# Kernel optimization log

Hardware: AMD Instinct MI355X
Metric: run time of the kernel (lower is better)

## Reference

```python
import jax, jax.numpy as jnp
import numpy as np
import math

NUM_WORDS = 8192
WORD_WIDTH = 512
PROJ_WIDTH = 64
NUM_HEADS = 8
SCALE_FACTOR = 100.0

def setup_inputs() -> dict:
    key = jax.random.key(0)
    kx, kq, kk, kv, ko = jax.random.split(key, 5)
    x = jax.random.normal(kx, (NUM_WORDS, WORD_WIDTH), dtype=jnp.float32)
    w_q = jax.random.normal(kq, (WORD_WIDTH, PROJ_WIDTH), dtype=jnp.float32) / SCALE_FACTOR
    w_k = jax.random.normal(kk, (WORD_WIDTH, PROJ_WIDTH), dtype=jnp.float32) / SCALE_FACTOR
    w_v = jax.random.normal(kv, (WORD_WIDTH, PROJ_WIDTH), dtype=jnp.float32) / SCALE_FACTOR
    w_o = jax.random.normal(ko, (WORD_WIDTH, WORD_WIDTH), dtype=jnp.float32)
    return {"x": x, "w_q": w_q, "w_k": w_k, "w_v": w_v, "w_o": w_o}

def reference(x, w_q, w_k, w_v, w_o):
    # Single self-attention head (all 8 heads in the source share the same weights).
    q = x @ w_q            # [N, P]
    k = x @ w_k            # [N, P]
    v = x @ w_v            # [N, P]
    scores = jax.nn.softmax((q @ k.T) / jnp.sqrt(jnp.float32(q.shape[1])), axis=1)  # [N, N]
    head = scores @ v      # [N, P]
    # concat of NUM_HEADS identical head outputs along dim=1
    concat = jnp.tile(head, (1, NUM_HEADS))  # [N, NUM_HEADS*P]
    return concat @ w_o    # [N, WORD_WIDTH]
```

## Files before the change

kernel.cpp:

```cpp
#include <hip/hip_runtime.h>
#include <stdint.h>

#define N_WORDS 8192
#define LOG2E_8 0.18033688011112043f

typedef __attribute__((ext_vector_type(8))) short short8;
typedef __attribute__((ext_vector_type(4))) float f32x4;
typedef __attribute__((ext_vector_type(16))) float f32x16;
typedef __attribute__((ext_vector_type(2))) __fp16 pkhalf2;
typedef __attribute__((ext_vector_type(4))) _Float16 half4;
typedef __attribute__((ext_vector_type(8))) _Float16 half8;

__device__ __forceinline__ unsigned short f32_to_bf16(float f) {
    union { float f; unsigned u; } v; v.f = f;
    unsigned u = v.u;
    return (unsigned short)((u + 0x7FFFu + ((u >> 16) & 1u)) >> 16);
}

__device__ __forceinline__ unsigned short f32_to_f16(float f) {
    union { _Float16 h; unsigned short u; } cv;
    cv.h = (_Float16)f;
    return cv.u;
}

__device__ __forceinline__ void async16(const void* g, void* l) {
    __builtin_amdgcn_global_load_lds(
        (const __attribute__((address_space(1))) unsigned int*)g,
        (__attribute__((address_space(3))) unsigned int*)l, 16, 0, 0);
}

__global__ __launch_bounds__(256) void qkv_gemm(
    const float* __restrict__ x,
    const float* __restrict__ wq, const float* __restrict__ wk,
    const float* __restrict__ wv, const float* __restrict__ wo,
    unsigned short* __restrict__ qB, unsigned short* __restrict__ kB,
    unsigned short* __restrict__ vH, unsigned short* __restrict__ weT)
{
    int t = threadIdx.x;
    int mat = blockIdx.y;

    if (mat == 3) {
        int i = blockIdx.x * 256 + t;
        int p = i >> 9;
        int j = i & 511;
        float s = 0.0f;
#pragma unroll
        for (int h = 0; h < 8; ++h) s += wo[(size_t)(h * 64 + p) * 512 + j];
        weT[(size_t)j * 64 + p] = f32_to_f16(s);
        return;
    }

    __shared__ __align__(16) unsigned short ldsX[64 * 72];
    __shared__ __align__(16) unsigned short ldsW[64 * 72];

    int mt = blockIdx.x;
    const float* w = (mat == 0) ? wq : (mat == 1) ? wk : wv;

    int wvid = t >> 6, lane = t & 63;
    int lq = lane & 15, quad = lane >> 4;

    f32x4 acc[4];
#pragma unroll
    for (int nt = 0; nt < 4; ++nt) acc[nt] = (f32x4){0.f, 0.f, 0.f, 0.f};

    float4 xr[4];
    float wr[16];
    int wn = t & 63, wkbs = (t >> 6) * 16;

    {
#pragma unroll
        for (int j2 = 0; j2 < 4; ++j2) {
            int i = t + j2 * 256;
            int row = i >> 4, c4 = (i & 15) * 4;
            xr[j2] = *(const float4*)(x + (size_t)(mt * 64 + row) * 512 + c4);
        }
#pragma unroll
        for (int kk = 0; kk < 16; ++kk)
            wr[kk] = w[(size_t)(wkbs + kk) * 64 + wn];
    }

    for (int kb = 0; kb < 8; ++kb) {
        __syncthreads();
#pragma unroll
        for (int j2 = 0; j2 < 4; ++j2) {
            int i = t + j2 * 256;
            int row = i >> 4, c4 = (i & 15) * 4;
            unsigned p0 = f32_to_bf16(xr[j2].x) | ((unsigned)f32_to_bf16(xr[j2].y) << 16);
            unsigned p1 = f32_to_bf16(xr[j2].z) | ((unsigned)f32_to_bf16(xr[j2].w) << 16);
            *(uint2*)(&ldsX[row * 72 + c4]) = make_uint2(p0, p1);
        }
#pragma unroll
        for (int kk = 0; kk < 16; kk += 2) {
            unsigned p = f32_to_bf16(wr[kk]) | ((unsigned)f32_to_bf16(wr[kk + 1]) << 16);
            *(unsigned*)(&ldsW[wn * 72 + wkbs + kk]) = p;
        }
        __syncthreads();

        if (kb < 7) {
            int k0 = (kb + 1) * 64;
#pragma unroll
            for (int j2 = 0; j2 < 4; ++j2) {
                int i = t + j2 * 256;
                int row = i >> 4, c4 = (i & 15) * 4;
                xr[j2] = *(const float4*)(x + (size_t)(mt * 64 + row) * 512 + k0 + c4);
            }
#pragma unroll
            for (int kk = 0; kk < 16; ++kk)
                wr[kk] = w[(size_t)(k0 + wkbs + kk) * 64 + wn];
        }

        int m = wvid * 16 + lq;
        short8 a0 = *(const short8*)(&ldsX[m * 72 + quad * 8]);
        short8 a1 = *(const short8*)(&ldsX[m * 72 + 32 + quad * 8]);
#pragma unroll
        for (int nt = 0; nt < 4; ++nt) {
            short8 b0 = *(const short8*)(&ldsW[(nt * 16 + lq) * 72 + quad * 8]);
            short8 b1 = *(const short8*)(&ldsW[(nt * 16 + lq) * 72 + 32 + quad * 8]);
            acc[nt] = __builtin_amdgcn_mfma_f32_16x16x32_bf16(a0, b0, acc[nt], 0, 0, 0);
            acc[nt] = __builtin_amdgcn_mfma_f32_16x16x32_bf16(a1, b1, acc[nt], 0, 0, 0);
        }
    }

    int mrow_base = mt * 64 + wvid * 16;
#pragma unroll
    for (int nt = 0; nt < 4; ++nt) {
#pragma unroll
        for (int r = 0; r < 4; ++r) {
            int row = mrow_base + quad * 4 + r;
            int n = nt * 16 + lq;
            float v = acc[nt][r];
            if (mat == 0) {
                v *= LOG2E_8;
                int col = ((((n >> 3) ^ (row & 7)) << 3)) | (n & 7);
                qB[(size_t)row * 64 + col] = f32_to_bf16(v);
            } else if (mat == 1) {
                int col = ((((n >> 3) ^ (row & 7)) << 3)) | (n & 7);
                kB[(size_t)row * 64 + col] = f32_to_bf16(v);
            } else {
                int rs = (row & ~63) | (((((row >> 3) & 7) ^ (n & 7)) << 3)) | (row & 7);
                vH[(size_t)n * N_WORDS + rs] = f32_to_f16(v);
            }
        }
    }
}

__global__ __launch_bounds__(256) void attn_kernel(
    const unsigned short* __restrict__ qB,
    const unsigned short* __restrict__ kB,
    const unsigned short* __restrict__ vH,
    unsigned short* __restrict__ pOh, float* __restrict__ pl,
    int nk, int sshift)
{
    __shared__ __align__(16) unsigned short ldsK[2][128 * 64];
    __shared__ __align__(16) unsigned short ldsV[2][64 * 128];

    int t = threadIdx.x;
    int bid = blockIdx.x;
    int s = bid & ((1 << sshift) - 1);
    int qb = bid >> sshift;
    int wvid = t >> 6, lane = t & 63;
    int l31 = lane & 31, hi = lane >> 5;
    int mbase = qb * 128 + wvid * 32;
    int n0 = s * nk;

    short8 qf[4];
    {
        int qrow = mbase + l31;
        const unsigned short* qr = qB + (size_t)qrow * 64;
        int s7 = qrow & 7;
#pragma unroll
        for (int c = 0; c < 4; ++c)
            qf[c] = *(const short8*)(qr + (((2 * c + hi) ^ s7) << 3));
    }

    f32x16 zero16;
#pragma unroll
    for (int i = 0; i < 16; ++i) zero16[i] = 0.f;
    f32x16 oacc[2];
    oacc[0] = zero16;
    oacc[1] = zero16;
    float lsum = 0.f;

    auto stage = [&](int buf, int nb) {
        const char* gK = (const char*)kB + (size_t)nb * 128;
#pragma unroll
        for (int i = 0; i < 4; ++i) {
            int L0 = (wvid * 4 + i) * 64;
            async16(gK + (size_t)(L0 + lane) * 16, (char*)ldsK[buf] + (size_t)L0 * 16);
        }
#pragma unroll
        for (int i = 0; i < 4; ++i) {
            int L0 = (wvid * 4 + i) * 64;
            int L = L0 + lane;
            int vcol = L >> 4, ct = L & 15;
            const char* src = (const char*)vH + (size_t)vcol * 16384 +
                              (size_t)nb * 2 + ((ct >> 3) << 7) + ((ct & 7) << 4);
            async16(src, (char*)ldsV[buf] + (size_t)L0 * 16);
        }
    };

    int tiles = nk >> 7;
    stage(0, n0);
    int cur = 0;

    for (int tt = 0; tt < tiles; ++tt) {
        __syncthreads();
        if (tt + 1 < tiles) stage(cur ^ 1, n0 + (tt + 1) * 128);

        __builtin_amdgcn_s_setprio(1);
        const unsigned short* K = ldsK[cur];
        const unsigned short* V = ldsV[cur];

#pragma unroll
        for (int nt = 0; nt < 4; ++nt) {
            const unsigned short* kr = K + (nt * 32 + l31) * 64;
            int s7 = l31 & 7;
            f32x16 st = zero16;
#pragma unroll
            for (int c = 0; c < 4; ++c) {
                short8 a = *(const short8*)(kr + (((2 * c + hi) ^ s7) << 3));
                st = __builtin_amdgcn_mfma_f32_32x32x16_bf16(a, qf[c], st, 0, 0, 0);
            }

            union { half8 v8[2]; pkhalf2 v2[8]; } pa;
#pragma unroll
            for (int p = 0; p < 8; ++p) {
                float e0 = exp2f(st[2 * p]);
                float e1 = exp2f(st[2 * p + 1]);
                lsum += e0 + e1;
                pa.v2[p] = __builtin_amdgcn_cvt_pkrtz(e0, e1);
            }

#pragma unroll
            for (int m = 0; m < 2; ++m) {
                int c0 = 4 * nt + 2 * m;
                int c1 = c0 + 1;
#pragma unroll
                for (int vt = 0; vt < 2; ++vt) {
                    int vcol = vt * 32 + l31;
                    int cs0 = (c0 & 8) | ((c0 & 7) ^ (vcol & 7));
                    int cs1 = (c1 & 8) | ((c1 & 7) ^ (vcol & 7));
                    union { half8 v8; half4 v4[2]; } vb;
                    vb.v4[0] = *(const half4*)(V + vcol * 128 + (cs0 << 3) + hi * 4);
                    vb.v4[1] = *(const half4*)(V + vcol * 128 + (cs1 << 3) + hi * 4);
                    oacc[vt] = __builtin_amdgcn_mfma_f32_32x32x16_f16(
                        pa.v8[m], vb.v8, oacc[vt], 0, 0, 0);
                }
            }
        }
        __builtin_amdgcn_s_setprio(0);
        cur ^= 1;
    }

    lsum += __shfl_xor(lsum, 32);

    size_t obase = (size_t)s * N_WORDS;
    if (hi == 0) pl[obase + mbase + l31] = lsum;

    __syncthreads();
    unsigned short* ldsO = &ldsK[0][0];
#pragma unroll
    for (int vt = 0; vt < 2; ++vt)
#pragma unroll
        for (int r = 0; r < 16; ++r) {
            int lrow = wvid * 32 + (r & 3) + 8 * (r >> 2) + 4 * hi;
            ldsO[lrow * 64 + vt * 32 + l31] = f32_to_f16(oacc[vt][r]);
        }
    __syncthreads();
    {
        const uint4* U = (const uint4*)ldsO;
        uint4* G = (uint4*)(pOh + (obase + (size_t)qb * 128) * 64);
#pragma unroll
        for (int j = 0; j < 4; ++j)
            G[t + 256 * j] = U[t + 256 * j];
    }
}

__global__ __launch_bounds__(256) void out_kernel(
    const unsigned short* __restrict__ pOh, const float* __restrict__ pl,
    const unsigned short* __restrict__ weT, float* __restrict__ out, int S)
{
    __shared__ __align__(16) _Float16 ldsH[16 * 72];
    int t = threadIdx.x;
    int r0 = blockIdx.x * 16;
    const _Float16* pOf = (const _Float16*)pOh;

#pragma unroll
    for (int j = 0; j < 4; ++j) {
        int i = t + j * 256;
        int row = i >> 6, d = i & 63;
        float so = 0.f, sl = 0.f;
        for (int s = 0; s < S; ++s) {
            so += (float)pOf[((size_t)s * N_WORDS + r0 + row) * 64 + d];
            sl += pl[(size_t)s * N_WORDS + r0 + row];
        }
        ldsH[row * 72 + d] = (_Float16)(so / sl);
    }
    __syncthreads();

    int wv = t >> 6, lane = t & 63;
    int lq = lane & 15, quad = lane >> 4;

    half8 a0 = *(const half8*)(&ldsH[lq * 72 + quad * 8]);
    half8 a1 = *(const half8*)(&ldsH[lq * 72 + 32 + quad * 8]);
    const _Float16* wT = (const _Float16*)weT;

#pragma unroll
    for (int ntl = 0; ntl < 8; ++ntl) {
        int nt = wv * 8 + ntl;
        const _Float16* wrow = wT + (size_t)(nt * 16 + lq) * 64;
        half8 b0 = *(const half8*)(wrow + quad * 8);
        half8 b1 = *(const half8*)(wrow + 32 + quad * 8);
        f32x4 acc = (f32x4){0.f, 0.f, 0.f, 0.f};
        acc = __builtin_amdgcn_mfma_f32_16x16x32_f16(a0, b0, acc, 0, 0, 0);
        acc = __builtin_amdgcn_mfma_f32_16x16x32_f16(a1, b1, acc, 0, 0, 0);
#pragma unroll
        for (int r = 0; r < 4; ++r)
            out[(size_t)(r0 + quad * 4 + r) * 512 + nt * 16 + lq] = acc[r];
    }
}

extern "C" void kernel_launch(void* const* d_in, const int* in_sizes, int n_in,
                              void* d_out, int out_size, void* d_ws, size_t ws_size,
                              hipStream_t stream)
{
    const float* x  = (const float*)d_in[0];
    const float* wq = (const float*)d_in[1];
    const float* wk = (const float*)d_in[2];
    const float* wv = (const float*)d_in[3];
    const float* wo = (const float*)d_in[4];
    float* out = (float*)d_out;

    char* ws = (char*)d_ws;
    unsigned short* qB  = (unsigned short*)(ws);
    unsigned short* kB  = (unsigned short*)(ws + 1048576);
    unsigned short* vH  = (unsigned short*)(ws + 2097152);
    unsigned short* weT = (unsigned short*)(ws + 3145728);
    float* pl           = (float*)(ws + 3211264);
    unsigned short* pOh = (unsigned short*)(ws + 3735552);

    size_t base = 3735552;
    int S = (ws_size >= base + 8u * 1048576u) ? 8 : 4;
    int sshift = (S == 8) ? 3 : 2;
    int nk = N_WORDS / S;

    hipLaunchKernelGGL(qkv_gemm, dim3(128, 4), dim3(256), 0, stream,
                       x, wq, wk, wv, wo, qB, kB, vH, weT);
    hipLaunchKernelGGL(attn_kernel, dim3(64 * S), dim3(256), 0, stream,
                       qB, kB, vH, pOh, pl, nk, sshift);
    hipLaunchKernelGGL(out_kernel, dim3(512), dim3(256), 0, stream,
                       pOh, pl, weT, out, S);
}
```

Before: 129.8 us.

## Process two query groups per wave to reuse K/V tiles, raise key splits

Each wave in the attention kernel now handles 64 query rows, as two 32-row groups, instead of 32. Every K and V fragment read from LDS feeds two MFMAs, which halves LDS read traffic per query and gives more independent MFMAs to interleave. To keep the grid size, the key-split count rises to 16 when the workspace is large enough, so each block walks fewer key tiles. The cost is roughly doubled accumulator and Q register usage, and more partial results for the output kernel to combine.

```diff
diff --git a/kernel.cpp b/kernel.cpp
--- a/kernel.cpp
+++ b/kernel.cpp
@@ -144,7 +144,7 @@
     }
 }
 
-__global__ __launch_bounds__(256) void attn_kernel(
+__global__ __launch_bounds__(256, 2) void attn_kernel(
     const unsigned short* __restrict__ qB,
     const unsigned short* __restrict__ kB,
     const unsigned short* __restrict__ vH,
@@ -160,26 +160,27 @@
     int qb = bid >> sshift;
     int wvid = t >> 6, lane = t & 63;
     int l31 = lane & 31, hi = lane >> 5;
-    int mbase = qb * 128 + wvid * 32;
+    int mbase = qb * 256 + wvid * 64;
     int n0 = s * nk;
 
-    short8 qf[4];
-    {
-        int qrow = mbase + l31;
+    short8 qf[2][4];
+#pragma unroll
+    for (int qg = 0; qg < 2; ++qg) {
+        int qrow = mbase + qg * 32 + l31;
         const unsigned short* qr = qB + (size_t)qrow * 64;
         int s7 = qrow & 7;
 #pragma unroll
         for (int c = 0; c < 4; ++c)
-            qf[c] = *(const short8*)(qr + (((2 * c + hi) ^ s7) << 3));
+            qf[qg][c] = *(const short8*)(qr + (((2 * c + hi) ^ s7) << 3));
     }
 
     f32x16 zero16;
 #pragma unroll
     for (int i = 0; i < 16; ++i) zero16[i] = 0.f;
-    f32x16 oacc[2];
-    oacc[0] = zero16;
-    oacc[1] = zero16;
-    float lsum = 0.f;
+    f32x16 oacc[2][2];
+    oacc[0][0] = zero16; oacc[0][1] = zero16;
+    oacc[1][0] = zero16; oacc[1][1] = zero16;
+    float lsum0 = 0.f, lsum1 = 0.f;
 
     auto stage = [&](int buf, int nb) {
         const char* gK = (const char*)kB + (size_t)nb * 128;
@@ -215,20 +216,31 @@
         for (int nt = 0; nt < 4; ++nt) {
             const unsigned short* kr = K + (nt * 32 + l31) * 64;
             int s7 = l31 & 7;
-            f32x16 st = zero16;
-#pragma unroll
-            for (int c = 0; c < 4; ++c) {
-                short8 a = *(const short8*)(kr + (((2 * c + hi) ^ s7) << 3));
-                st = __builtin_amdgcn_mfma_f32_32x32x16_bf16(a, qf[c], st, 0, 0, 0);
-            }
-
-            union { half8 v8[2]; pkhalf2 v2[8]; } pa;
+            short8 a0 = *(const short8*)(kr + (((0 + hi) ^ s7) << 3));
+            short8 a1 = *(const short8*)(kr + (((2 + hi) ^ s7) << 3));
+            short8 a2 = *(const short8*)(kr + (((4 + hi) ^ s7) << 3));
+            short8 a3 = *(const short8*)(kr + (((6 + hi) ^ s7) << 3));
+            f32x16 st0 = zero16, st1 = zero16;
+            st0 = __builtin_amdgcn_mfma_f32_32x32x16_bf16(a0, qf[0][0], st0, 0, 0, 0);
+            st1 = __builtin_amdgcn_mfma_f32_32x32x16_bf16(a0, qf[1][0], st1, 0, 0, 0);
+            st0 = __builtin_amdgcn_mfma_f32_32x32x16_bf16(a1, qf[0][1], st0, 0, 0, 0);
+            st1 = __builtin_amdgcn_mfma_f32_32x32x16_bf16(a1, qf[1][1], st1, 0, 0, 0);
+            st0 = __builtin_amdgcn_mfma_f32_32x32x16_bf16(a2, qf[0][2], st0, 0, 0, 0);
+            st1 = __builtin_amdgcn_mfma_f32_32x32x16_bf16(a2, qf[1][2], st1, 0, 0, 0);
+            st0 = __builtin_amdgcn_mfma_f32_32x32x16_bf16(a3, qf[0][3], st0, 0, 0, 0);
+            st1 = __builtin_amdgcn_mfma_f32_32x32x16_bf16(a3, qf[1][3], st1, 0, 0, 0);
+
+            union { half8 v8[2]; pkhalf2 v2[8]; } pa0, pa1;
 #pragma unroll
             for (int p = 0; p < 8; ++p) {
-                float e0 = exp2f(st[2 * p]);
-                float e1 = exp2f(st[2 * p + 1]);
-                lsum += e0 + e1;
-                pa.v2[p] = __builtin_amdgcn_cvt_pkrtz(e0, e1);
+                float e0 = exp2f(st0[2 * p]);
+                float e1 = exp2f(st0[2 * p + 1]);
+                lsum0 += e0 + e1;
+                pa0.v2[p] = __builtin_amdgcn_cvt_pkrtz(e0, e1);
+                float f0 = exp2f(st1[2 * p]);
+                float f1 = exp2f(st1[2 * p + 1]);
+                lsum1 += f0 + f1;
+                pa1.v2[p] = __builtin_amdgcn_cvt_pkrtz(f0, f1);
             }
 
 #pragma unroll
@@ -243,8 +255,10 @@
                     union { half8 v8; half4 v4[2]; } vb;
                     vb.v4[0] = *(const half4*)(V + vcol * 128 + (cs0 << 3) + hi * 4);
                     vb.v4[1] = *(const half4*)(V + vcol * 128 + (cs1 << 3) + hi * 4);
-                    oacc[vt] = __builtin_amdgcn_mfma_f32_32x32x16_f16(
-                        pa.v8[m], vb.v8, oacc[vt], 0, 0, 0);
+                    oacc[0][vt] = __builtin_amdgcn_mfma_f32_32x32x16_f16(
+                        pa0.v8[m], vb.v8, oacc[0][vt], 0, 0, 0);
+                    oacc[1][vt] = __builtin_amdgcn_mfma_f32_32x32x16_f16(
+                        pa1.v8[m], vb.v8, oacc[1][vt], 0, 0, 0);
                 }
             }
         }
@@ -252,26 +266,32 @@
         cur ^= 1;
     }
 
-    lsum += __shfl_xor(lsum, 32);
+    lsum0 += __shfl_xor(lsum0, 32);
+    lsum1 += __shfl_xor(lsum1, 32);
 
     size_t obase = (size_t)s * N_WORDS;
-    if (hi == 0) pl[obase + mbase + l31] = lsum;
+    if (hi == 0) {
+        pl[obase + mbase + l31] = lsum0;
+        pl[obase + mbase + 32 + l31] = lsum1;
+    }
 
     __syncthreads();
     unsigned short* ldsO = &ldsK[0][0];
 #pragma unroll
-    for (int vt = 0; vt < 2; ++vt)
-#pragma unroll
-        for (int r = 0; r < 16; ++r) {
-            int lrow = wvid * 32 + (r & 3) + 8 * (r >> 2) + 4 * hi;
-            ldsO[lrow * 64 + vt * 32 + l31] = f32_to_f16(oacc[vt][r]);
-        }
+    for (int qg = 0; qg < 2; ++qg)
+#pragma unroll
+        for (int vt = 0; vt < 2; ++vt)
+#pragma unroll
+            for (int r = 0; r < 16; ++r) {
+                int lrow = wvid * 64 + qg * 32 + (r & 3) + 8 * (r >> 2) + 4 * hi;
+                ldsO[lrow * 64 + vt * 32 + l31] = f32_to_f16(oacc[qg][vt][r]);
+            }
     __syncthreads();
     {
         const uint4* U = (const uint4*)ldsO;
-        uint4* G = (uint4*)(pOh + (obase + (size_t)qb * 128) * 64);
-#pragma unroll
-        for (int j = 0; j < 4; ++j)
+        uint4* G = (uint4*)(pOh + (obase + (size_t)qb * 256) * 64);
+#pragma unroll
+        for (int j = 0; j < 8; ++j)
             G[t + 256 * j] = U[t + 256 * j];
     }
 }
@@ -340,13 +360,15 @@
     unsigned short* pOh = (unsigned short*)(ws + 3735552);
 
     size_t base = 3735552;
-    int S = (ws_size >= base + 8u * 1048576u) ? 8 : 4;
-    int sshift = (S == 8) ? 3 : 2;
+    int S, sshift;
+    if (ws_size >= base + 16u * 1048576u) { S = 16; sshift = 4; }
+    else                                  { S = 8;  sshift = 3; }
     int nk = N_WORDS / S;
+    int nqb = N_WORDS / 256;
 
     hipLaunchKernelGGL(qkv_gemm, dim3(128, 4), dim3(256), 0, stream,
                        x, wq, wk, wv, wo, qB, kB, vH, weT);
-    hipLaunchKernelGGL(attn_kernel, dim3(64 * S), dim3(256), 0, stream,
+    hipLaunchKernelGGL(attn_kernel, dim3(nqb * S), dim3(256), 0, stream,
                        qB, kB, vH, pOh, pl, nk, sshift);
     hipLaunchKernelGGL(out_kernel, dim3(512), dim3(256), 0, stream,
                        pOh, pl, weT, out, S);
```

New measurement: 145.6 us. 12.1% more time.

## Pre-pack K and V in MFMA fragment order for contiguous tile loads

Applied to the files above, without the earlier changes.

The projection kernel now writes K and V into a blocked layout where each 128-key tile is a contiguous 16KB chunk already arranged in per-lane MFMA operand order. Staging becomes a straight linear copy of K and V, and the inner loop reads each operand as one 16-byte LDS load at a lane-linear address. This replaces the XOR-swizzled addressing and the paired 8-byte V reads. The aim is to cut address arithmetic and LDS instruction count and to make the global V loads coalesced, at the cost of a more complex scatter in the projection store.

```diff
diff --git a/kernel.cpp b/kernel.cpp
--- a/kernel.cpp
+++ b/kernel.cpp
@@ -134,11 +134,24 @@
                 int col = ((((n >> 3) ^ (row & 7)) << 3)) | (n & 7);
                 qB[(size_t)row * 64 + col] = f32_to_bf16(v);
             } else if (mat == 1) {
-                int col = ((((n >> 3) ^ (row & 7)) << 3)) | (n & 7);
-                kB[(size_t)row * 64 + col] = f32_to_bf16(v);
+                int c2 = n >> 3;
+                int j  = n & 7;
+                size_t addr = (size_t)(row >> 7) * 8192
+                            + (size_t)((((row >> 5) & 3) << 2) + (c2 >> 1)) * 512
+                            + (size_t)(((c2 & 1) << 5) + (row & 31)) * 8 + j;
+                kB[addr] = f32_to_bf16(v);
             } else {
-                int rs = (row & ~63) | (((((row >> 3) & 7) ^ (n & 7)) << 3)) | (row & 7);
-                vH[(size_t)n * N_WORDS + rs] = f32_to_f16(v);
+                int kt  = row & 127;
+                int nt2 = kt >> 5;
+                int k32 = kt & 31;
+                int m2  = k32 >> 4;
+                int k16 = k32 & 15;
+                int hi2 = (k16 >> 2) & 1;
+                int j2  = (k16 & 3) | ((k16 >> 3) << 2);
+                size_t addr = (size_t)(row >> 7) * 8192
+                            + (size_t)((((nt2 << 1) + m2) << 1) + (n >> 5)) * 512
+                            + (size_t)((hi2 << 5) + (n & 31)) * 8 + j2;
+                vH[addr] = f32_to_f16(v);
             }
         }
     }
@@ -182,20 +195,13 @@
     float lsum = 0.f;
 
     auto stage = [&](int buf, int nb) {
-        const char* gK = (const char*)kB + (size_t)nb * 128;
+        const char* gK = (const char*)kB + (size_t)(nb >> 7) * 16384;
+        const char* gV = (const char*)vH + (size_t)(nb >> 7) * 16384;
 #pragma unroll
         for (int i = 0; i < 4; ++i) {
             int L0 = (wvid * 4 + i) * 64;
             async16(gK + (size_t)(L0 + lane) * 16, (char*)ldsK[buf] + (size_t)L0 * 16);
-        }
-#pragma unroll
-        for (int i = 0; i < 4; ++i) {
-            int L0 = (wvid * 4 + i) * 64;
-            int L = L0 + lane;
-            int vcol = L >> 4, ct = L & 15;
-            const char* src = (const char*)vH + (size_t)vcol * 16384 +
-                              (size_t)nb * 2 + ((ct >> 3) << 7) + ((ct & 7) << 4);
-            async16(src, (char*)ldsV[buf] + (size_t)L0 * 16);
+            async16(gV + (size_t)(L0 + lane) * 16, (char*)ldsV[buf] + (size_t)L0 * 16);
         }
     };
 
@@ -208,17 +214,15 @@
         if (tt + 1 < tiles) stage(cur ^ 1, n0 + (tt + 1) * 128);
 
         __builtin_amdgcn_s_setprio(1);
-        const unsigned short* K = ldsK[cur];
-        const unsigned short* V = ldsV[cur];
+        const char* Kb = (const char*)ldsK[cur] + (size_t)lane * 16;
+        const char* Vb = (const char*)ldsV[cur] + (size_t)lane * 16;
 
 #pragma unroll
         for (int nt = 0; nt < 4; ++nt) {
-            const unsigned short* kr = K + (nt * 32 + l31) * 64;
-            int s7 = l31 & 7;
             f32x16 st = zero16;
 #pragma unroll
             for (int c = 0; c < 4; ++c) {
-                short8 a = *(const short8*)(kr + (((2 * c + hi) ^ s7) << 3));
+                short8 a = *(const short8*)(Kb + (nt * 4 + c) * 1024);
                 st = __builtin_amdgcn_mfma_f32_32x32x16_bf16(a, qf[c], st, 0, 0, 0);
             }
 
@@ -233,18 +237,11 @@
 
 #pragma unroll
             for (int m = 0; m < 2; ++m) {
-                int c0 = 4 * nt + 2 * m;
-                int c1 = c0 + 1;
 #pragma unroll
                 for (int vt = 0; vt < 2; ++vt) {
-                    int vcol = vt * 32 + l31;
-                    int cs0 = (c0 & 8) | ((c0 & 7) ^ (vcol & 7));
-                    int cs1 = (c1 & 8) | ((c1 & 7) ^ (vcol & 7));
-                    union { half8 v8; half4 v4[2]; } vb;
-                    vb.v4[0] = *(const half4*)(V + vcol * 128 + (cs0 << 3) + hi * 4);
-                    vb.v4[1] = *(const half4*)(V + vcol * 128 + (cs1 << 3) + hi * 4);
+                    half8 vb = *(const half8*)(Vb + (((nt * 2 + m) * 2) + vt) * 1024);
                     oacc[vt] = __builtin_amdgcn_mfma_f32_32x32x16_f16(
-                        pa.v8[m], vb.v8, oacc[vt], 0, 0, 0);
+                        pa.v8[m], vb, oacc[vt], 0, 0, 0);
                 }
             }
         }
```

After: 125.6 us. -3.3%, faster.
